# Kernel optimization log

Measured on AMD Instinct MI355X. Metric: run time of the kernel, lower is better.

The kernel has to match this reference:

```python
import jax, jax.numpy as jnp
import numpy as np

X_DIM, R_DIM, U_DIM, V_DIM, H_DIM = 64, 64, 64, 64, 128


def setup_inputs() -> dict:
    key = jax.random.key(0)
    k1, k2, k3, k4, k5 = jax.random.split(key, 5)
    n, i, j = 8, 32, 32
    r = jax.random.normal(k1, (n, i, j, R_DIM), dtype=jnp.float32)
    u = jax.random.normal(k2, (n, R_DIM, U_DIM, V_DIM), dtype=jnp.float32)
    v = jax.random.normal(k3, (n, i, j, V_DIM), dtype=jnp.float32)
    # xavier_uniform scaling: gain=1, fan computed over last two dims per torch default
    def xavier(k, shape):
        fan_in, fan_out = shape[-1], shape[-2]
        # torch xavier on >2D tensor: fan_in = shape[1]*prod(shape[2:]), fan_out = shape[0]*prod(shape[2:])
        rf = int(np.prod(shape[2:])) if len(shape) > 2 else 1
        fi = shape[1] * rf
        fo = shape[0] * rf
        bound = float(np.sqrt(6.0 / (fi + fo)))
        return jax.random.uniform(k, shape, dtype=jnp.float32, minval=-bound, maxval=bound)
    w1 = xavier(k4, (R_DIM, U_DIM, V_DIM, H_DIM))
    w2 = xavier(k5, (X_DIM, R_DIM, H_DIM))
    return {"r": r, "u": u, "v": v, "w1": w1, "w2": w2}


def reference(r, u, v, w1, w2):
    # contract w1 with u over (u_dim, v_dim) -> per-batch tensor a[n, r, v', h]
    # original: einsum('ruvh,nruv,nijv->nijrh')
    a = jnp.einsum('ruvh,nruv->nrvh', w1, u)          # contract u axis; v survives? no:
    # Careful: in 'ruvh,nruv,nijv->nijrh', v is contracted across all three.
    # Do it in two GEMM-friendly steps: first contract u-axis, keeping v.
    # a: [n, r, v, h] (contracted only over u)
    a = jnp.einsum('ruvh,nruv->nrvh', w1, u)
    # then contract v with v-tensor: [n,i,j,v] x [n,r,v,h] -> [n,i,j,r,h]
    x = jax.nn.relu(jnp.einsum('nijv,nrvh->nijrh', v, a))
    # second einsum: 'xrh,nijr,nijrh->nijx'
    # fuse r-weighting into x first (elementwise over r), then contract (r,h) with w2
    out = jnp.einsum('xrh,nijrh->nijx', w2, x * r[..., None])
    return out
```

## Files before the change

### kernel.cpp

```cpp
#include <hip/hip_runtime.h>
#include <hip/hip_bf16.h>

#define RD 64
#define UD 64
#define VD 64
#define HD 128
#define XD 64
#define NB 8
#define SITES 1024

typedef float f32x4 __attribute__((ext_vector_type(4)));
typedef __bf16 bf16x4 __attribute__((ext_vector_type(4)));
typedef __bf16 bf16x8 __attribute__((ext_vector_type(8)));
typedef unsigned int u32x4 __attribute__((ext_vector_type(4)));
typedef unsigned short u16;
typedef unsigned short u16x4 __attribute__((ext_vector_type(4)));

__device__ __forceinline__ void lds_barrier() {
  __builtin_amdgcn_s_waitcnt(0xC07F);
  __builtin_amdgcn_s_barrier();
}

__global__ void kprep(const float* __restrict__ w2, u16* __restrict__ w2t,
                      const float* __restrict__ r, float* __restrict__ rt,
                      const float* __restrict__ u, float* __restrict__ ut) {
  __shared__ float tl[64][68];
  int b = blockIdx.x;
  int t = threadIdx.x;
  if (b < 256) {
    int rr = b >> 2, qq = b & 3;
    for (int i = 0; i < 8; ++i) {
      int idx = qq * 2048 + i * 256 + t;
      int x = idx >> 7, h = idx & 127;
      float val = w2[((size_t)x * RD + rr) * HD + h];
      __hip_bfloat16 hv = __float2bfloat16(val);
      w2t[((size_t)rr * XD + x) * HD + h] = *(u16*)&hv;
    }
  } else if (b < 384) {
    int bb = b - 256;
    int n = bb >> 4, sb = (bb & 15) * 64;
    for (int i = 0; i < 4; ++i) {
      int flat = i * 256 + t;
      int s = flat >> 4, ch = flat & 15;
      f32x4 d = *(const f32x4*)(r + ((size_t)(n * SITES + sb + s) * RD + ch * 4));
      *(f32x4*)&tl[s][ch * 4] = d;
    }
    __syncthreads();
    for (int i = 0; i < 4; ++i) {
      int flat = i * 256 + t;
      int rr = flat >> 4, ch = flat & 15;
      f32x4 o;
      o.x = tl[ch * 4 + 0][rr];
      o.y = tl[ch * 4 + 1][rr];
      o.z = tl[ch * 4 + 2][rr];
      o.w = tl[ch * 4 + 3][rr];
      *(f32x4*)(rt + ((size_t)(n * RD + rr) * SITES + sb + ch * 4)) = o;
    }
  } else {
    int f = (b - 384) * 256 + t;
    int nh = f & 1, v = (f >> 1) & 63, uu = (f >> 7) & 63, rr = f >> 13;
    f32x4 o;
#pragma unroll
    for (int k = 0; k < 4; ++k)
      o[k] = u[(((size_t)(nh * 4 + k) * RD + rr) * UD + uu) * VD + v];
    *(f32x4*)(ut + (size_t)f * 4) = o;
  }
}

__global__ __launch_bounds__(256, 2) void k_a_full(const float* __restrict__ w1,
                                                   const float* __restrict__ ut,
                                                   u16* __restrict__ at) {
  __shared__ float tile[32][34];
  int b = blockIdx.x;
  int rr = b >> 3, vh = (b >> 2) & 1, hb = b & 3;
  int t = threadIdx.x;
  int vl = t >> 3, hs = t & 7;
  int v = vh * 32 + vl;
  int h0 = hb * 32 + hs * 4;
  const float* w1p = w1 + ((size_t)(rr * UD) * VD + v) * HD + h0;
  const float* up  = ut + ((size_t)(rr * UD) * VD + v) * NB;

  float acc[8][4];
#pragma unroll
  for (int n = 0; n < 8; ++n)
#pragma unroll
    for (int j = 0; j < 4; ++j) acc[n][j] = 0.f;

#pragma unroll 4
  for (int uu = 0; uu < 64; ++uu) {
    f32x4 wv = *(const f32x4*)(w1p + (size_t)uu * (VD * HD));
    f32x4 a0 = *(const f32x4*)(up + (size_t)uu * (VD * NB));
    f32x4 a1 = *(const f32x4*)(up + (size_t)uu * (VD * NB) + 4);
    float un[8];
    un[0] = a0.x; un[1] = a0.y; un[2] = a0.z; un[3] = a0.w;
    un[4] = a1.x; un[5] = a1.y; un[6] = a1.z; un[7] = a1.w;
#pragma unroll
    for (int n = 0; n < 8; ++n)
#pragma unroll
      for (int j = 0; j < 4; ++j) acc[n][j] += un[n] * wv[j];
  }

  int hl = t >> 3, vs = t & 7;
  for (int n = 0; n < 8; ++n) {
    __syncthreads();
#pragma unroll
    for (int j = 0; j < 4; ++j) tile[hs * 4 + j][vl] = acc[n][j];
    __syncthreads();
    f32x4 blk = *(const f32x4*)&tile[hl][vs * 4];
    u16x4 o;
#pragma unroll
    for (int j = 0; j < 4; ++j) {
      __hip_bfloat16 hv = __float2bfloat16(blk[j]);
      o[j] = *(u16*)&hv;
    }
    *(u16x4*)(at + ((size_t)(n * RD + rr) * HD + hb * 32 + hl) * VD + vh * 32 + vs * 4) = o;
  }
}

__global__ __launch_bounds__(256, 1) void k_main(const float* __restrict__ vin,
                                                 const u16* __restrict__ at,
                                                 const u16* __restrict__ w2t,
                                                 const float* __restrict__ rt,
                                                 float* __restrict__ pbuf) {
  __shared__ __align__(16) char Plds[2 * 128 * 256];
  int b = blockIdx.x;
  int rc = b & 7, st = (b >> 3) & 7, n = b >> 6;
  int t = threadIdx.x;
  int w = t >> 6, L = t & 63, q = L >> 4, c = L & 15;
  int g2m = w >> 1, g2x = w & 1;

  bf16x8 vf[4][2];
#pragma unroll
  for (int nt = 0; nt < 4; ++nt)
#pragma unroll
    for (int ks = 0; ks < 2; ++ks) {
      int s = (w & 1) * 64 + nt * 16 + c;
      const float* vp = vin + ((size_t)(n * SITES + st * 128 + s) * VD + ks * 32 + q * 8);
      f32x4 a0 = *(const f32x4*)vp;
      f32x4 a1 = *(const f32x4*)(vp + 4);
      bf16x8 f;
      f[0] = (__bf16)a0.x; f[1] = (__bf16)a0.y; f[2] = (__bf16)a0.z; f[3] = (__bf16)a0.w;
      f[4] = (__bf16)a1.x; f[5] = (__bf16)a1.y; f[6] = (__bf16)a1.z; f[7] = (__bf16)a1.w;
      vf[nt][ks] = f;
    }

  f32x4 o[4][2];
#pragma unroll
  for (int i = 0; i < 4; i++)
#pragma unroll
    for (int j = 0; j < 2; j++) o[i][j] = (f32x4)0.f;

  int g1m = w >> 1, g1n = w & 1;
  for (int rr = rc * 8; rr < rc * 8 + 8; ++rr) {
    const u16* abase = at + (size_t)(n * RD + rr) * 8192;

    bf16x8 af[4][2];
#pragma unroll
    for (int mt = 0; mt < 4; ++mt)
#pragma unroll
      for (int ks = 0; ks < 2; ++ks) {
        int h = g1m * 64 + mt * 16 + c;
        int vb = ks * 4 + q;
        af[mt][ks] = *(const bf16x8*)(abase + (size_t)h * VD + vb * 8);
      }
    u32x4 wraw[2][4];
#pragma unroll
    for (int xt = 0; xt < 2; ++xt)
#pragma unroll
      for (int k2 = 0; k2 < 4; ++k2) {
        int xg = g2x * 32 + xt * 16 + c;
        wraw[xt][k2] = *(const u32x4*)((const char*)w2t +
                        (((size_t)(rr * XD + xg)) * HD + k2 * 32 + q * 8) * 2);
      }
    float rsc[4];
#pragma unroll
    for (int nt = 0; nt < 4; ++nt)
      rsc[nt] = rt[(size_t)(n * RD + rr) * SITES + st * 128 + g1n * 64 + nt * 16 + c];

    f32x4 cc[4][4];
#pragma unroll
    for (int mt = 0; mt < 4; ++mt)
#pragma unroll
      for (int nt = 0; nt < 4; ++nt) cc[mt][nt] = (f32x4)0.f;
#pragma unroll
    for (int ks = 0; ks < 2; ++ks)
#pragma unroll
      for (int mt = 0; mt < 4; ++mt)
#pragma unroll
        for (int nt = 0; nt < 4; ++nt)
          cc[mt][nt] = __builtin_amdgcn_mfma_f32_16x16x32_bf16(af[mt][ks], vf[nt][ks],
                                                               cc[mt][nt], 0, 0, 0);

    char* PB = Plds + (rr & 1) * 32768;
#pragma unroll
    for (int mt = 0; mt < 4; ++mt)
#pragma unroll
      for (int nt = 0; nt < 4; ++nt) {
        float sc = rsc[nt];
        bf16x4 pv;
#pragma unroll
        for (int jj = 0; jj < 4; ++jj) {
          float x = cc[mt][nt][jj];
          x = x > 0.f ? x : 0.f;
          pv[jj] = (__bf16)(x * sc);
        }
        int s = g1n * 64 + nt * 16 + c;
        int blk = g1m * 8 + mt * 2 + (q >> 1);
        *(bf16x4*)(PB + (size_t)s * 256 + (size_t)((blk ^ c) * 16 + (q & 1) * 8)) = pv;
      }
    lds_barrier();

#pragma unroll
    for (int k2 = 0; k2 < 4; ++k2) {
      bf16x8 wf0 = __builtin_bit_cast(bf16x8, wraw[0][k2]);
      bf16x8 wf1 = __builtin_bit_cast(bf16x8, wraw[1][k2]);
#pragma unroll
      for (int mt = 0; mt < 4; ++mt) {
        int s = g2m * 64 + mt * 16 + c;
        int blk = k2 * 4 + q;
        bf16x8 pf = *(const bf16x8*)(PB + (size_t)s * 256 + (size_t)((blk ^ c) * 16));
        o[mt][0] = __builtin_amdgcn_mfma_f32_16x16x32_bf16(pf, wf0, o[mt][0], 0, 0, 0);
        o[mt][1] = __builtin_amdgcn_mfma_f32_16x16x32_bf16(pf, wf1, o[mt][1], 0, 0, 0);
      }
    }
  }
#pragma unroll
  for (int mt = 0; mt < 4; ++mt)
#pragma unroll
    for (int xt = 0; xt < 2; ++xt) {
      int s0 = g2m * 64 + mt * 16 + q * 4;
      int x = g2x * 32 + xt * 16 + c;
      size_t off = ((((size_t)rc * NB + n) * 8 + st) * XD + x) * 128 + s0;
      *(f32x4*)(pbuf + off) = o[mt][xt];
    }
}

__global__ __launch_bounds__(256) void k_reduce(const float* __restrict__ pbuf,
                                                float* __restrict__ out) {
  __shared__ float tile[128][17];
  int b = blockIdx.x;
  int n = b >> 5, st = (b >> 2) & 7, xq = b & 3;
  int t = threadIdx.x;
  int sq = t & 31, xl = t >> 5;
#pragma unroll
  for (int p = 0; p < 2; ++p) {
    int x = xq * 16 + p * 8 + xl;
    f32x4 sum = (f32x4)0.f;
#pragma unroll
    for (int rcc = 0; rcc < 8; ++rcc) {
      size_t off = ((((size_t)rcc * NB + n) * 8 + st) * XD + x) * 128 + sq * 4;
      f32x4 d = *(const f32x4*)(pbuf + off);
      sum.x += d.x; sum.y += d.y; sum.z += d.z; sum.w += d.w;
    }
#pragma unroll
    for (int k = 0; k < 4; ++k) tile[sq * 4 + k][p * 8 + xl] = sum[k];
  }
  __syncthreads();
#pragma unroll
  for (int k = 0; k < 2; ++k) {
    int flat = k * 256 + t;
    int s = flat >> 2, c4 = flat & 3;
    f32x4 o;
#pragma unroll
    for (int j = 0; j < 4; ++j) o[j] = tile[s][c4 * 4 + j];
    *(f32x4*)(out + ((size_t)(n * SITES + st * 128 + s) * XD + xq * 16 + c4 * 4)) = o;
  }
}

extern "C" void kernel_launch(void* const* d_in, const int* in_sizes, int n_in,
                              void* d_out, int out_size, void* d_ws, size_t ws_size,
                              hipStream_t stream) {
  const float* r  = (const float*)d_in[0];
  const float* u  = (const float*)d_in[1];
  const float* v  = (const float*)d_in[2];
  const float* w1 = (const float*)d_in[3];
  const float* w2 = (const float*)d_in[4];
  float* out = (float*)d_out;
  char* ws = (char*)d_ws;
  u16* at     = (u16*)(ws);
  u16* w2t    = (u16*)(ws + ((size_t)8 << 20));
  float* rt   = (float*)(ws + ((size_t)9 << 20));
  float* ut   = (float*)(ws + ((size_t)11 << 20));
  float* pbuf = (float*)(ws + ((size_t)19 << 20));

  hipLaunchKernelGGL(kprep, dim3(2432), dim3(256), 0, stream, w2, w2t, r, rt, u, ut);
  hipLaunchKernelGGL(k_a_full, dim3(512), dim3(256), 0, stream, w1, ut, at);
  hipLaunchKernelGGL(k_main, dim3(512), dim3(256), 0, stream, v, at, w2t, rt, pbuf);
  hipLaunchKernelGGL(k_reduce, dim3(256), dim3(256), 0, stream, pbuf, out);
}
```

Before: 260.0 us.

## Restructure k_a_full with 1024-thread blocks, batch-split threads and register prefetch

Rewrites the w1·u contraction kernel to use 256 blocks of 1024 threads. Each thread computes 2 batches × 8 h-values instead of 8 batches × 4 h-values, and the w1/u loads are software-prefetched PF=4 iterations ahead in registers. The output transpose now goes through one large LDS tile with a single barrier instead of eight barrier pairs. The aim is to raise parallelism and memory-level overlap in this prep stage, at the cost of higher LDS use and w1 being re-read by the four batch-group waves.

```diff
diff --git a/kernel.cpp b/kernel.cpp
--- a/kernel.cpp
+++ b/kernel.cpp
@@ -10,6 +10,7 @@
 #define SITES 1024
 
 typedef float f32x4 __attribute__((ext_vector_type(4)));
+typedef float f32x2 __attribute__((ext_vector_type(2)));
 typedef __bf16 bf16x4 __attribute__((ext_vector_type(4)));
 typedef __bf16 bf16x8 __attribute__((ext_vector_type(8)));
 typedef unsigned int u32x4 __attribute__((ext_vector_type(4)));
@@ -67,53 +68,77 @@
   }
 }
 
-__global__ __launch_bounds__(256, 2) void k_a_full(const float* __restrict__ w1,
-                                                   const float* __restrict__ ut,
-                                                   u16* __restrict__ at) {
-  __shared__ float tile[32][34];
+#define PF 4
+__global__ __launch_bounds__(1024, 4) void k_a_full(const float* __restrict__ w1,
+                                                    const float* __restrict__ ut,
+                                                    u16* __restrict__ at) {
+  __shared__ float tile[8 * 64 * 40];
   int b = blockIdx.x;
-  int rr = b >> 3, vh = (b >> 2) & 1, hb = b & 3;
+  int rr = b >> 2, vh = (b >> 1) & 1, hb = b & 1;
   int t = threadIdx.x;
-  int vl = t >> 3, hs = t & 7;
+  int ng = t >> 8;
+  int L = t & 255;
+  int vl = L >> 3, hs = L & 7;
   int v = vh * 32 + vl;
-  int h0 = hb * 32 + hs * 4;
-  const float* w1p = w1 + ((size_t)(rr * UD) * VD + v) * HD + h0;
-  const float* up  = ut + ((size_t)(rr * UD) * VD + v) * NB;
-
-  float acc[8][4];
-#pragma unroll
-  for (int n = 0; n < 8; ++n)
-#pragma unroll
-    for (int j = 0; j < 4; ++j) acc[n][j] = 0.f;
-
-#pragma unroll 4
+  int h0 = hb * 64 + hs * 8;
+  int n0 = ng * 2;
+  const float* w1p = w1 + (((size_t)rr * UD) * VD + v) * HD + h0;
+  const float* up  = ut + (((size_t)rr * UD) * VD + v) * NB + n0;
+  const size_t wstep = (size_t)VD * HD;
+  const size_t ustep = (size_t)VD * NB;
+
+  float acc[2][8];
+#pragma unroll
+  for (int nn = 0; nn < 2; ++nn)
+#pragma unroll
+    for (int j = 0; j < 8; ++j) acc[nn][j] = 0.f;
+
+  f32x4 wa[PF], wb[PF];
+  f32x2 ub[PF];
+#pragma unroll
+  for (int p = 0; p < PF; ++p) {
+    wa[p] = *(const f32x4*)(w1p + (size_t)p * wstep);
+    wb[p] = *(const f32x4*)(w1p + (size_t)p * wstep + 4);
+    ub[p] = *(const f32x2*)(up + (size_t)p * ustep);
+  }
+#pragma unroll
   for (int uu = 0; uu < 64; ++uu) {
-    f32x4 wv = *(const f32x4*)(w1p + (size_t)uu * (VD * HD));
-    f32x4 a0 = *(const f32x4*)(up + (size_t)uu * (VD * NB));
-    f32x4 a1 = *(const f32x4*)(up + (size_t)uu * (VD * NB) + 4);
-    float un[8];
-    un[0] = a0.x; un[1] = a0.y; un[2] = a0.z; un[3] = a0.w;
-    un[4] = a1.x; un[5] = a1.y; un[6] = a1.z; un[7] = a1.w;
-#pragma unroll
-    for (int n = 0; n < 8; ++n)
-#pragma unroll
-      for (int j = 0; j < 4; ++j) acc[n][j] += un[n] * wv[j];
-  }
-
-  int hl = t >> 3, vs = t & 7;
-  for (int n = 0; n < 8; ++n) {
-    __syncthreads();
-#pragma unroll
-    for (int j = 0; j < 4; ++j) tile[hs * 4 + j][vl] = acc[n][j];
-    __syncthreads();
-    f32x4 blk = *(const f32x4*)&tile[hl][vs * 4];
+    const int p = uu & (PF - 1);
+    f32x4 w0 = wa[p];
+    f32x4 w1v = wb[p];
+    f32x2 uv = ub[p];
+    if (uu + PF < 64) {
+      wa[p] = *(const f32x4*)(w1p + (size_t)(uu + PF) * wstep);
+      wb[p] = *(const f32x4*)(w1p + (size_t)(uu + PF) * wstep + 4);
+      ub[p] = *(const f32x2*)(up + (size_t)(uu + PF) * ustep);
+    }
+#pragma unroll
+    for (int j = 0; j < 4; ++j) {
+      acc[0][j]     += uv.x * w0[j];
+      acc[0][j + 4] += uv.x * w1v[j];
+      acc[1][j]     += uv.y * w0[j];
+      acc[1][j + 4] += uv.y * w1v[j];
+    }
+  }
+
+#pragma unroll
+  for (int nn = 0; nn < 2; ++nn)
+#pragma unroll
+    for (int j = 0; j < 8; ++j)
+      tile[((n0 + nn) * 64 + hs * 8 + j) * 40 + vl] = acc[nn][j];
+  __syncthreads();
+#pragma unroll
+  for (int k = 0; k < 4; ++k) {
+    int uidx = k * 1024 + t;
+    int n = uidx >> 9, hl = (uidx >> 3) & 63, vs = uidx & 7;
+    f32x4 blk = *(const f32x4*)&tile[(n * 64 + hl) * 40 + vs * 4];
     u16x4 o;
 #pragma unroll
     for (int j = 0; j < 4; ++j) {
       __hip_bfloat16 hv = __float2bfloat16(blk[j]);
       o[j] = *(u16*)&hv;
     }
-    *(u16x4*)(at + ((size_t)(n * RD + rr) * HD + hb * 32 + hl) * VD + vh * 32 + vs * 4) = o;
+    *(u16x4*)(at + ((size_t)(n * RD + rr) * HD + hb * 64 + hl) * VD + vh * 32 + vs * 4) = o;
   }
 }
 
@@ -284,7 +309,7 @@
   float* pbuf = (float*)(ws + ((size_t)19 << 20));
 
   hipLaunchKernelGGL(kprep, dim3(2432), dim3(256), 0, stream, w2, w2t, r, rt, u, ut);
-  hipLaunchKernelGGL(k_a_full, dim3(512), dim3(256), 0, stream, w1, ut, at);
+  hipLaunchKernelGGL(k_a_full, dim3(256), dim3(1024), 0, stream, w1, ut, at);
   hipLaunchKernelGGL(k_main, dim3(512), dim3(256), 0, stream, v, at, w2t, rt, pbuf);
   hipLaunchKernelGGL(k_reduce, dim3(256), dim3(256), 0, stream, pbuf, out);
 }
```

Measured after the change: 302.2 us. +16.2%, slower.

## Split u-contraction across two half-blocks with LDS reduction and register prefetch

Applied to the files above, without the earlier changes.

The w1·u contraction kernel now runs 512 threads per block, with each half covering 32 of the 64 u values. Partial sums are combined through a swizzled LDS buffer, and the loads are software-pipelined with a 4-deep register prefetch ring. The transpose now stages all 8 batches in one LDS tile and writes them out after a single barrier, replacing per-batch double syncs. The aim is more memory-level parallelism and fewer barriers in this bandwidth-bound stage, at the cost of more LDS (~66KB per block), which may limit occupancy.

```diff
diff --git a/kernel.cpp b/kernel.cpp
--- a/kernel.cpp
+++ b/kernel.cpp
@@ -10,6 +10,7 @@
 #define SITES 1024
 
 typedef float f32x4 __attribute__((ext_vector_type(4)));
+typedef float f32x2 __attribute__((ext_vector_type(2)));
 typedef __bf16 bf16x4 __attribute__((ext_vector_type(4)));
 typedef __bf16 bf16x8 __attribute__((ext_vector_type(8)));
 typedef unsigned int u32x4 __attribute__((ext_vector_type(4)));
@@ -67,46 +68,80 @@
   }
 }
 
-__global__ __launch_bounds__(256, 2) void k_a_full(const float* __restrict__ w1,
+#define PF 4
+__global__ __launch_bounds__(512, 4) void k_a_full(const float* __restrict__ w1,
                                                    const float* __restrict__ ut,
                                                    u16* __restrict__ at) {
-  __shared__ float tile[32][34];
+  __shared__ float red[256 * 32];
+  __shared__ float tile[8 * 32 * 33];
   int b = blockIdx.x;
   int rr = b >> 3, vh = (b >> 2) & 1, hb = b & 3;
   int t = threadIdx.x;
-  int vl = t >> 3, hs = t & 7;
+  int uh = t >> 8;
+  int L = t & 255;
+  int vl = L >> 3, hs = L & 7;
   int v = vh * 32 + vl;
   int h0 = hb * 32 + hs * 4;
-  const float* w1p = w1 + ((size_t)(rr * UD) * VD + v) * HD + h0;
-  const float* up  = ut + ((size_t)(rr * UD) * VD + v) * NB;
-
-  float acc[8][4];
-#pragma unroll
-  for (int n = 0; n < 8; ++n)
-#pragma unroll
-    for (int j = 0; j < 4; ++j) acc[n][j] = 0.f;
-
-#pragma unroll 4
-  for (int uu = 0; uu < 64; ++uu) {
-    f32x4 wv = *(const f32x4*)(w1p + (size_t)uu * (VD * HD));
-    f32x4 a0 = *(const f32x4*)(up + (size_t)uu * (VD * NB));
-    f32x4 a1 = *(const f32x4*)(up + (size_t)uu * (VD * NB) + 4);
-    float un[8];
-    un[0] = a0.x; un[1] = a0.y; un[2] = a0.z; un[3] = a0.w;
-    un[4] = a1.x; un[5] = a1.y; un[6] = a1.z; un[7] = a1.w;
+  const float* w1p = w1 + (((size_t)(rr * UD + uh * 32)) * VD + v) * HD + h0;
+  const float* up  = ut + (((size_t)(rr * UD + uh * 32)) * VD + v) * NB;
+  const size_t wstep = (size_t)VD * HD;
+  const size_t ustep = (size_t)VD * NB;
+
+  f32x4 acc[8];
+#pragma unroll
+  for (int n = 0; n < 8; ++n) acc[n] = (f32x4)0.f;
+
+  f32x4 wa[PF], ua[PF], ub[PF];
+#pragma unroll
+  for (int p = 0; p < PF; ++p) {
+    wa[p] = *(const f32x4*)(w1p + (size_t)p * wstep);
+    ua[p] = *(const f32x4*)(up + (size_t)p * ustep);
+    ub[p] = *(const f32x4*)(up + (size_t)p * ustep + 4);
+  }
+#pragma unroll
+  for (int uu = 0; uu < 32; ++uu) {
+    const int p = uu & (PF - 1);
+    f32x4 wv = wa[p];
+    f32x4 a0 = ua[p];
+    f32x4 a1 = ub[p];
+    if (uu + PF < 32) {
+      wa[p] = *(const f32x4*)(w1p + (size_t)(uu + PF) * wstep);
+      ua[p] = *(const f32x4*)(up + (size_t)(uu + PF) * ustep);
+      ub[p] = *(const f32x4*)(up + (size_t)(uu + PF) * ustep + 4);
+    }
+    acc[0] += wv * a0.x;
+    acc[1] += wv * a0.y;
+    acc[2] += wv * a0.z;
+    acc[3] += wv * a0.w;
+    acc[4] += wv * a1.x;
+    acc[5] += wv * a1.y;
+    acc[6] += wv * a1.z;
+    acc[7] += wv * a1.w;
+  }
+
+  if (uh == 1) {
 #pragma unroll
     for (int n = 0; n < 8; ++n)
-#pragma unroll
-      for (int j = 0; j < 4; ++j) acc[n][j] += un[n] * wv[j];
-  }
-
-  int hl = t >> 3, vs = t & 7;
-  for (int n = 0; n < 8; ++n) {
-    __syncthreads();
-#pragma unroll
-    for (int j = 0; j < 4; ++j) tile[hs * 4 + j][vl] = acc[n][j];
-    __syncthreads();
-    f32x4 blk = *(const f32x4*)&tile[hl][vs * 4];
+      *(f32x4*)&red[L * 32 + ((n ^ (L & 7)) << 2)] = acc[n];
+  }
+  __syncthreads();
+  if (uh == 0) {
+#pragma unroll
+    for (int n = 0; n < 8; ++n)
+      acc[n] += *(const f32x4*)&red[L * 32 + ((n ^ (L & 7)) << 2)];
+#pragma unroll
+    for (int n = 0; n < 8; ++n)
+#pragma unroll
+      for (int j = 0; j < 4; ++j)
+        tile[(n * 32 + hs * 4 + j) * 33 + vl] = acc[n][j];
+  }
+  __syncthreads();
+
+#pragma unroll
+  for (int k = 0; k < 4; ++k) {
+    int flat = k * 512 + t;
+    int vs = flat & 7, hl = (flat >> 3) & 31, n = flat >> 8;
+    f32x4 blk = *(const f32x4*)&tile[(n * 32 + hl) * 33 + vs * 4];
     u16x4 o;
 #pragma unroll
     for (int j = 0; j < 4; ++j) {
@@ -284,7 +319,7 @@
   float* pbuf = (float*)(ws + ((size_t)19 << 20));
 
   hipLaunchKernelGGL(kprep, dim3(2432), dim3(256), 0, stream, w2, w2t, r, rt, u, ut);
-  hipLaunchKernelGGL(k_a_full, dim3(512), dim3(256), 0, stream, w1, ut, at);
+  hipLaunchKernelGGL(k_a_full, dim3(512), dim3(512), 0, stream, w1, ut, at);
   hipLaunchKernelGGL(k_main, dim3(512), dim3(256), 0, stream, v, at, w2t, rt, pbuf);
   hipLaunchKernelGGL(k_reduce, dim3(256), dim3(256), 0, stream, pbuf, out);
 }
```

Result: no change. 255.3 us (-1.8%).

## Register-prefetch w1/u loads in k_a_full and widen per-thread h tile

Applied to the files above, without the earlier changes.

Reworks the w1×u contraction kernel so each thread computes 8 h values instead of 4, and uses an 8-deep register ring to prefetch w1 and u loads several u-iterations ahead. The transpose epilogue now stages all 8 batches in one large LDS tile with a single barrier, replacing the per-batch double barriers. The grid is halved to 256 blocks at one block per CU. The aim is to hide global load latency and cut sync overhead, at the cost of higher register pressure and lower occupancy.

```diff
diff --git a/kernel.cpp b/kernel.cpp
--- a/kernel.cpp
+++ b/kernel.cpp
@@ -10,6 +10,7 @@
 #define SITES 1024
 
 typedef float f32x4 __attribute__((ext_vector_type(4)));
+typedef float f32x2 __attribute__((ext_vector_type(2)));
 typedef __bf16 bf16x4 __attribute__((ext_vector_type(4)));
 typedef __bf16 bf16x8 __attribute__((ext_vector_type(8)));
 typedef unsigned int u32x4 __attribute__((ext_vector_type(4)));
@@ -67,53 +68,89 @@
   }
 }
 
-__global__ __launch_bounds__(256, 2) void k_a_full(const float* __restrict__ w1,
+#define PF 8
+__global__ __launch_bounds__(256, 1) void k_a_full(const float* __restrict__ w1,
                                                    const float* __restrict__ ut,
                                                    u16* __restrict__ at) {
-  __shared__ float tile[32][34];
+  __shared__ float tile[8 * 128 * 17];
   int b = blockIdx.x;
-  int rr = b >> 3, vh = (b >> 2) & 1, hb = b & 3;
+  int rr = b >> 2, vq = b & 3;
   int t = threadIdx.x;
-  int vl = t >> 3, hs = t & 7;
-  int v = vh * 32 + vl;
-  int h0 = hb * 32 + hs * 4;
-  const float* w1p = w1 + ((size_t)(rr * UD) * VD + v) * HD + h0;
-  const float* up  = ut + ((size_t)(rr * UD) * VD + v) * NB;
-
-  float acc[8][4];
+  int vl = t >> 4;
+  int hs = t & 15;
+  int v = vq * 16 + vl;
+  int h0 = hs * 8;
+  const float* w1p = w1 + ((size_t)rr * UD * VD + v) * HD + h0;
+  const float* up  = ut + ((size_t)rr * UD * VD + v) * NB;
+
+  f32x4 accA[8], accB[8];
+#pragma unroll
+  for (int n = 0; n < 8; ++n) { accA[n] = (f32x4)0.f; accB[n] = (f32x4)0.f; }
+
+  f32x4 wa[PF], wb[PF], ua[PF], ub[PF];
+#pragma unroll
+  for (int p = 0; p < PF; ++p) {
+    wa[p] = *(const f32x4*)(w1p + (size_t)p * 8192);
+    wb[p] = *(const f32x4*)(w1p + (size_t)p * 8192 + 4);
+    ua[p] = *(const f32x4*)(up + (size_t)p * 512);
+    ub[p] = *(const f32x4*)(up + (size_t)p * 512 + 4);
+  }
+
+#define KA_CONSUME(P)                                                     \
+  {                                                                       \
+    f32x4 w0 = wa[P], w1v = wb[P], u0 = ua[P], u1 = ub[P];                \
+    accA[0] += w0 * u0.x; accB[0] += w1v * u0.x;                          \
+    accA[1] += w0 * u0.y; accB[1] += w1v * u0.y;                          \
+    accA[2] += w0 * u0.z; accB[2] += w1v * u0.z;                          \
+    accA[3] += w0 * u0.w; accB[3] += w1v * u0.w;                          \
+    accA[4] += w0 * u1.x; accB[4] += w1v * u1.x;                          \
+    accA[5] += w0 * u1.y; accB[5] += w1v * u1.y;                          \
+    accA[6] += w0 * u1.z; accB[6] += w1v * u1.z;                          \
+    accA[7] += w0 * u1.w; accB[7] += w1v * u1.w;                          \
+  }
+
+#pragma unroll 8
+  for (int uu = 0; uu < 56; ++uu) {
+    const int p = uu & 7;
+    f32x4 w0 = wa[p], w1v = wb[p], u0 = ua[p], u1 = ub[p];
+    wa[p] = *(const f32x4*)(w1p + (size_t)(uu + 8) * 8192);
+    wb[p] = *(const f32x4*)(w1p + (size_t)(uu + 8) * 8192 + 4);
+    ua[p] = *(const f32x4*)(up + (size_t)(uu + 8) * 512);
+    ub[p] = *(const f32x4*)(up + (size_t)(uu + 8) * 512 + 4);
+    accA[0] += w0 * u0.x; accB[0] += w1v * u0.x;
+    accA[1] += w0 * u0.y; accB[1] += w1v * u0.y;
+    accA[2] += w0 * u0.z; accB[2] += w1v * u0.z;
+    accA[3] += w0 * u0.w; accB[3] += w1v * u0.w;
+    accA[4] += w0 * u1.x; accB[4] += w1v * u1.x;
+    accA[5] += w0 * u1.y; accB[5] += w1v * u1.y;
+    accA[6] += w0 * u1.z; accB[6] += w1v * u1.z;
+    accA[7] += w0 * u1.w; accB[7] += w1v * u1.w;
+  }
+  KA_CONSUME(0) KA_CONSUME(1) KA_CONSUME(2) KA_CONSUME(3)
+  KA_CONSUME(4) KA_CONSUME(5) KA_CONSUME(6) KA_CONSUME(7)
+#undef KA_CONSUME
+
 #pragma unroll
   for (int n = 0; n < 8; ++n)
 #pragma unroll
-    for (int j = 0; j < 4; ++j) acc[n][j] = 0.f;
-
-#pragma unroll 4
-  for (int uu = 0; uu < 64; ++uu) {
-    f32x4 wv = *(const f32x4*)(w1p + (size_t)uu * (VD * HD));
-    f32x4 a0 = *(const f32x4*)(up + (size_t)uu * (VD * NB));
-    f32x4 a1 = *(const f32x4*)(up + (size_t)uu * (VD * NB) + 4);
-    float un[8];
-    un[0] = a0.x; un[1] = a0.y; un[2] = a0.z; un[3] = a0.w;
-    un[4] = a1.x; un[5] = a1.y; un[6] = a1.z; un[7] = a1.w;
-#pragma unroll
-    for (int n = 0; n < 8; ++n)
-#pragma unroll
-      for (int j = 0; j < 4; ++j) acc[n][j] += un[n] * wv[j];
-  }
-
-  int hl = t >> 3, vs = t & 7;
-  for (int n = 0; n < 8; ++n) {
-    __syncthreads();
-#pragma unroll
-    for (int j = 0; j < 4; ++j) tile[hs * 4 + j][vl] = acc[n][j];
-    __syncthreads();
-    f32x4 blk = *(const f32x4*)&tile[hl][vs * 4];
+    for (int j = 0; j < 4; ++j) {
+      tile[((n << 7) + h0 + j) * 17 + vl] = accA[n][j];
+      tile[((n << 7) + h0 + 4 + j) * 17 + vl] = accB[n][j];
+    }
+  __syncthreads();
+
+#pragma unroll
+  for (int k = 0; k < 16; ++k) {
+    int flat = k * 256 + t;
+    int c4 = flat & 3, h = (flat >> 2) & 127, n = flat >> 9;
+    const float* src = &tile[((n << 7) + h) * 17 + c4 * 4];
     u16x4 o;
 #pragma unroll
     for (int j = 0; j < 4; ++j) {
-      __hip_bfloat16 hv = __float2bfloat16(blk[j]);
+      __hip_bfloat16 hv = __float2bfloat16(src[j]);
       o[j] = *(u16*)&hv;
     }
-    *(u16x4*)(at + ((size_t)(n * RD + rr) * HD + hb * 32 + hl) * VD + vh * 32 + vs * 4) = o;
+    *(u16x4*)(at + (((size_t)n * RD + rr) * HD + h) * VD + vq * 16 + c4 * 4) = o;
   }
 }
 
@@ -284,7 +321,7 @@
   float* pbuf = (float*)(ws + ((size_t)19 << 20));
 
   hipLaunchKernelGGL(kprep, dim3(2432), dim3(256), 0, stream, w2, w2t, r, rt, u, ut);
-  hipLaunchKernelGGL(k_a_full, dim3(512), dim3(256), 0, stream, w1, ut, at);
+  hipLaunchKernelGGL(k_a_full, dim3(256), dim3(256), 0, stream, w1, ut, at);
   hipLaunchKernelGGL(k_main, dim3(512), dim3(256), 0, stream, v, at, w2t, rt, pbuf);
   hipLaunchKernelGGL(k_reduce, dim3(256), dim3(256), 0, stream, pbuf, out);
 }
```

After: 259.6 us. Within noise of the previous version (-0.2%).
